# Kernel optimization log

Hardware: AMD Instinct MI355X
Metric: run time of the kernel (lower is better)

The kernel has to match this reference:

```python
import jax, jax.numpy as jnp
import numpy as np

D_MODEL = 512
N_HEADS = 8
D_HEAD = 64
D_FF = 1024
EPS = 1e-5


def setup_inputs() -> dict:
    key = jax.random.key(0)
    ks = jax.random.split(key, 9)
    B, L = 4, 2048
    s = lambda fan_in: 1.0 / np.sqrt(fan_in)
    return {
        "x": jax.random.normal(ks[0], (B, L, D_MODEL), dtype=jnp.float32),
        "ln1_w": jnp.ones((D_MODEL,), jnp.float32),
        "ln1_b": jnp.zeros((D_MODEL,), jnp.float32),
        "ln2_w": jnp.ones((D_MODEL,), jnp.float32),
        "ln2_b": jnp.zeros((D_MODEL,), jnp.float32),
        "wq": jax.random.normal(ks[1], (D_MODEL, N_HEADS * D_HEAD), jnp.float32) * s(D_MODEL),
        "wk": jax.random.normal(ks[2], (D_MODEL, N_HEADS * D_HEAD), jnp.float32) * s(D_MODEL),
        "wv": jax.random.normal(ks[3], (D_MODEL, N_HEADS * D_HEAD), jnp.float32) * s(D_MODEL),
        "wo": jax.random.normal(ks[4], (N_HEADS * D_HEAD, D_MODEL), jnp.float32) * s(N_HEADS * D_HEAD),
        "w_gate": jax.random.normal(ks[5], (D_MODEL, D_FF), jnp.float32) * s(D_MODEL),
        "w_up": jax.random.normal(ks[6], (D_MODEL, D_FF), jnp.float32) * s(D_MODEL),
        "w_down": jax.random.normal(ks[7], (D_FF, D_MODEL), jnp.float32) * s(D_FF),
    }


def _layernorm(x, w, b):
    mu = jnp.mean(x, axis=-1, keepdims=True)
    var = jnp.var(x, axis=-1, keepdims=True)
    return (x - mu) * jax.lax.rsqrt(var + EPS) * w + b


def reference(x, ln1_w, ln1_b, ln2_w, ln2_b, wq, wk, wv, wo, w_gate, w_up, w_down):
    B, L, _ = x.shape
    scale = D_HEAD ** -0.5

    # --- attention sublayer (pre-LN residual) ---
    h = _layernorm(x, ln1_w, ln1_b)
    q = (h @ wq).reshape(B, L, N_HEADS, D_HEAD)  # [B,L,H,Dh]
    k = (h @ wk).reshape(B, L, N_HEADS, D_HEAD)
    v = (h @ wv).reshape(B, L, N_HEADS, D_HEAD)
    scores = jnp.einsum("bqhd,bkhd->bhqk", q, k) * scale
    # softmax computed in fp32, cast back (matches F.softmax(dtype=float32).to(q.dtype))
    attn = jax.nn.softmax(scores.astype(jnp.float32), axis=-1).astype(q.dtype)
    out = jnp.einsum("bhqk,bkhd->bqhd", attn, v).reshape(B, L, N_HEADS * D_HEAD)
    x = x + out @ wo

    # --- SwiGLU FFN sublayer (pre-LN residual) ---
    h = _layernorm(x, ln2_w, ln2_b)
    gate = jax.nn.silu(h @ w_gate)
    x = x + (gate * (h @ w_up)) @ w_down
    return x
```

## Files before the change

### kernel.cpp

```cpp
#include <hip/hip_runtime.h>
#include <hip/hip_bf16.h>
#include <math.h>

#define EPS 1e-5f

typedef __attribute__((ext_vector_type(8))) short bf16x8;
typedef __attribute__((ext_vector_type(4))) float f32x4;
typedef __attribute__((ext_vector_type(16))) float f32x16;

#define MFMA16 __builtin_amdgcn_mfma_f32_16x16x32_bf16
#define MFMA32 __builtin_amdgcn_mfma_f32_32x32x16_bf16

__device__ __forceinline__ short f2bf(float x) {
    union { float f; unsigned u; } un; un.f = x;
    unsigned r = un.u + 0x7FFF + ((un.u >> 16) & 1);
    return (short)(r >> 16);
}
__device__ __forceinline__ float bf2f(short s) {
    union { unsigned u; float f; } un;
    un.u = ((unsigned)(unsigned short)s) << 16;
    return un.f;
}
__device__ __forceinline__ unsigned pack_bf2(float a, float b) {
    unsigned r;
    asm("v_cvt_pk_bf16_f32 %0, %1, %2" : "=v"(r) : "v"(a), "v"(b));
    return r;
}
__device__ __forceinline__ float exp2_fast(float x) {
    float r;
    asm("v_exp_f32 %0, %1" : "=v"(r) : "v"(x));
    return r;
}
__device__ __forceinline__ void permswap(unsigned& a, unsigned& b) {
    asm volatile("v_permlane32_swap_b32 %0, %1" : "+v"(a), "+v"(b));
}
__device__ __forceinline__ bf16x8 mk_frag(unsigned a, unsigned b, unsigned c, unsigned d) {
    union { unsigned u[4]; bf16x8 v; } t;
    t.u[0] = a; t.u[1] = b; t.u[2] = c; t.u[3] = d;
    return t.v;
}
__device__ __forceinline__ void load_lds16(const short* g, short* l) {
    __builtin_amdgcn_global_load_lds(
        (const __attribute__((address_space(1))) unsigned int*)g,
        (__attribute__((address_space(3))) unsigned int*)l, 16, 0, 0);
}
__device__ __forceinline__ void wait_vm0_barrier() {
    asm volatile("s_waitcnt vmcnt(0)" ::: "memory");
    __builtin_amdgcn_s_barrier();
    __builtin_amdgcn_sched_barrier(0);
}

__global__ __launch_bounds__(256) void ln_kernel_b(const float* __restrict__ in,
                                                   const float* __restrict__ w,
                                                   const float* __restrict__ bb,
                                                   short* __restrict__ out) {
    int wv = threadIdx.x >> 6, lane = threadIdx.x & 63;
    int row = blockIdx.x * 4 + wv;
    const float* x = in + (size_t)row * 512 + lane * 8;
    float4 v0 = *(const float4*)x;
    float4 v1 = *(const float4*)(x + 4);
    float s  = (v0.x + v0.y) + (v0.z + v0.w) + (v1.x + v1.y) + (v1.z + v1.w);
    float s2 = v0.x*v0.x + v0.y*v0.y + v0.z*v0.z + v0.w*v0.w
             + v1.x*v1.x + v1.y*v1.y + v1.z*v1.z + v1.w*v1.w;
#pragma unroll
    for (int off = 1; off < 64; off <<= 1) {
        s  += __shfl_xor(s, off);
        s2 += __shfl_xor(s2, off);
    }
    float mu = s * (1.f / 512.f);
    float rstd = rsqrtf(s2 * (1.f / 512.f) - mu * mu + EPS);
    const float4 wa = *(const float4*)&w[lane * 8];
    const float4 wb = *(const float4*)&w[lane * 8 + 4];
    const float4 ba = *(const float4*)&bb[lane * 8];
    const float4 bv = *(const float4*)&bb[lane * 8 + 4];
    uint4 o;
    o.x = pack_bf2((v0.x - mu) * rstd * wa.x + ba.x, (v0.y - mu) * rstd * wa.y + ba.y);
    o.y = pack_bf2((v0.z - mu) * rstd * wa.z + ba.z, (v0.w - mu) * rstd * wa.w + ba.w);
    o.z = pack_bf2((v1.x - mu) * rstd * wb.x + bv.x, (v1.y - mu) * rstd * wb.y + bv.y);
    o.w = pack_bf2((v1.z - mu) * rstd * wb.z + bv.z, (v1.w - mu) * rstd * wb.w + bv.w);
    *(uint4*)&out[(size_t)row * 512 + lane * 8] = o;
}

struct WT { const float* w; short* t; int K; int N; };
struct WT7 { WT a[7]; };
__global__ __launch_bounds__(256) void transp_w_kernel(WT7 p) {
    WT e = p.a[blockIdx.z];
    int k0 = blockIdx.x * 32, n0 = blockIdx.y * 32;
    if (k0 >= e.K || n0 >= e.N) return;
    __shared__ short t[32][33];
    int tx = threadIdx.x & 31, ty = threadIdx.x >> 5;
#pragma unroll
    for (int pp = 0; pp < 4; pp++)
        t[pp * 8 + ty][tx] = f2bf(e.w[(size_t)(k0 + pp * 8 + ty) * e.N + n0 + tx]);
    __syncthreads();
#pragma unroll
    for (int pp = 0; pp < 4; pp++)
        e.t[(size_t)(n0 + pp * 8 + ty) * e.K + k0 + tx] = t[tx][pp * 8 + ty];
}

template <int EPI, int BM, int BN>
__global__ __launch_bounds__(256) void gemm_mfma(const short* __restrict__ A,
                                                 const short* __restrict__ Bt,
                                                 const float* __restrict__ res,
                                                 const short* __restrict__ resb,
                                                 void* __restrict__ Cv,
                                                 int M, int N, int K) {
    constexpr int MI = BM >> 5;
    constexpr int NJ = BN >> 5;
    __shared__ short As[2][BM * 64];
    __shared__ short Bs[2][BN * 64];
    const int tid = threadIdx.x;
    const int lane = tid & 63, w = tid >> 6;
    const int g = lane >> 4, r16 = lane & 15;
    const int wr = w >> 1, wc = w & 1;

    const int nb = gridDim.x * gridDim.y;
    const int fid = blockIdx.y * gridDim.x + blockIdx.x;
    const int nid = (fid & 7) * (nb >> 3) + (fid >> 3);
    const int m0 = (nid / gridDim.x) * BM, n0 = (nid % gridDim.x) * BN;

    const int lr = lane >> 3;
    const int ck = (lane & 7) ^ lr;

    auto stage = [&](int buf, int k0) {
#pragma unroll
        for (int p = 0; p < BM / 32; p++) {
            int rb = w * (BM / 4) + p * 8;
            load_lds16(&A[(size_t)(m0 + rb + lr) * K + k0 + ck * 8], &As[buf][rb * 64]);
        }
#pragma unroll
        for (int p = 0; p < BN / 32; p++) {
            int rb = w * (BN / 4) + p * 8;
            load_lds16(&Bt[(size_t)(n0 + rb + lr) * K + k0 + ck * 8], &Bs[buf][rb * 64]);
        }
    };

    f32x4 acc[MI][NJ] = {};
    stage(0, 0);
    wait_vm0_barrier();

    const int nt = K >> 6;
    int cur = 0;
    for (int t = 0; t < nt; t++) {
        if (t + 1 < nt) stage(cur ^ 1, (t + 1) << 6);
#pragma unroll
        for (int ks = 0; ks < 2; ks++) {
            bf16x8 av[MI], bv[NJ];
#pragma unroll
            for (int i = 0; i < MI; i++) {
                int row = wr * (BM >> 1) + i * 16 + r16;
                av[i] = *(const bf16x8*)&As[cur][row * 64 + ((ks * 4 + g) ^ (row & 7)) * 8];
            }
#pragma unroll
            for (int j = 0; j < NJ; j++) {
                int row = wc * (BN >> 1) + j * 16 + r16;
                bv[j] = *(const bf16x8*)&Bs[cur][row * 64 + ((ks * 4 + g) ^ (row & 7)) * 8];
            }
#pragma unroll
            for (int i = 0; i < MI; i++)
#pragma unroll
                for (int j = 0; j < NJ; j++)
                    acc[i][j] = MFMA16(av[i], bv[j], acc[i][j], 0, 0, 0);
        }
        wait_vm0_barrier();
        cur ^= 1;
    }

#pragma unroll
    for (int i = 0; i < MI; i++)
#pragma unroll
        for (int j = 0; j < NJ; j++)
#pragma unroll
            for (int jr = 0; jr < 4; jr++) {
                int m = m0 + wr * (BM >> 1) + i * 16 + 4 * g + jr;
                int n = n0 + wc * (BN >> 1) + j * 16 + r16;
                float v = acc[i][j][jr];
                if (EPI == 0) {
                    size_t idx = (size_t)m * N + n;
                    ((float*)Cv)[idx] = res[idx] + v;
                } else if (EPI == 1) {
                    ((short*)Cv)[(size_t)m * N + n] = f2bf(v);
                } else if (EPI == 2) {
                    if (n < 512) v *= 0.18033688011112042f;
                    if (n < 1024) {
                        ((short*)Cv)[(size_t)(n >> 9) * 4194304 +
                                     (((size_t)(m >> 11) * 8 + ((n >> 6) & 7)) * 2048 + (m & 2047)) * 64 + (n & 63)] = f2bf(v);
                    } else {
                        ((short*)Cv)[(size_t)2 * 4194304 +
                                     (((size_t)(m >> 11) * 8 + ((n >> 6) & 7)) * 64 + (n & 63)) * 2048 + (m & 2047)] = f2bf(v);
                    }
                } else {
                    float gt = bf2f(resb[(size_t)m * N + n]);
                    float y = gt / (1.f + __expf(-gt)) * v;
                    ((short*)Cv)[(size_t)m * N + n] = f2bf(y);
                }
            }
}

__global__ __launch_bounds__(256) void attn_mfma_kernel(const short* __restrict__ qb,
                                                        const short* __restrict__ kb,
                                                        const short* __restrict__ vt,
                                                        short* __restrict__ outb) {
    __shared__ short SM[16384];

    const int fid = blockIdx.y * gridDim.x + blockIdx.x;
    const int nid = (fid & 7) * 64 + (fid >> 3);
    const int bh = nid >> 4, qt = nid & 15;
    const int b = bh >> 3, h = bh & 7;
    const int q0 = qt * 128;
    const size_t hb = (size_t)bh * (2048 * 64);

    const int tid = threadIdx.x;
    const int lane = tid & 63, w = tid >> 6;
    const int hi = lane >> 5;
    const int l31 = lane & 31;
    const int lr = lane >> 3, ck = (lane & 7) ^ lr;

#pragma unroll
    for (int p = 0; p < 4; p++)
        load_lds16(&qb[hb + (size_t)(q0 + 32 * w + 8 * p + lr) * 64 + ck * 8],
                   &SM[8192 + (32 * w + 8 * p) * 64]);
    wait_vm0_barrier();
    bf16x8 qf[4];
    {
        int row = 32 * w + l31;
#pragma unroll
        for (int ds = 0; ds < 4; ds++)
            qf[ds] = *(const bf16x8*)&SM[8192 + row * 64 + ((2 * ds + hi) ^ (row & 7)) * 8];
    }
    asm volatile("s_waitcnt lgkmcnt(0)" ::: "memory");
    __builtin_amdgcn_s_barrier();
    __builtin_amdgcn_sched_barrier(0);

    auto stageKV = [&](int buf, int kt) {
        int k0 = kt * 64;
        int rb = w * 16;
        short* Kd = &SM[buf * 4096];
        short* Vd = &SM[8192 + buf * 4096];
        load_lds16(&kb[hb + (size_t)(k0 + rb + lr) * 64 + ck * 8],       &Kd[rb * 64]);
        load_lds16(&kb[hb + (size_t)(k0 + rb + 8 + lr) * 64 + ck * 8],   &Kd[(rb + 8) * 64]);
        load_lds16(&vt[hb + (size_t)(rb + lr) * 2048 + k0 + ck * 8],     &Vd[rb * 64]);
        load_lds16(&vt[hb + (size_t)(rb + 8 + lr) * 2048 + k0 + ck * 8], &Vd[(rb + 8) * 64]);
    };
    stageKV(0, 0);
    wait_vm0_barrier();

    float m_ = -1e30f, l_ = 0.f;
    f32x16 o0 = (f32x16)(0.f), o1 = (f32x16)(0.f);
    int cur = 0;

    for (int t = 0; t < 32; t++) {
        if (t + 1 < 32) stageKV(cur ^ 1, t + 1);
        const short* Kc = &SM[cur * 4096];
        const short* Vc = &SM[8192 + cur * 4096];

        f32x16 s0 = (f32x16)(0.f), s1 = (f32x16)(0.f);
        {
            int r0 = l31, r1 = 32 + l31;
            int cshift = (l31 & 7);
#pragma unroll
            for (int ds = 0; ds < 4; ds++) {
                bf16x8 k0f = *(const bf16x8*)&Kc[r0 * 64 + ((2 * ds + hi) ^ cshift) * 8];
                bf16x8 k1f = *(const bf16x8*)&Kc[r1 * 64 + ((2 * ds + hi) ^ cshift) * 8];
                s0 = MFMA32(k0f, qf[ds], s0, 0, 0, 0);
                s1 = MFMA32(k1f, qf[ds], s1, 0, 0, 0);
            }
        }

        float q0m = fmaxf(fmaxf(s0[0], s0[1]),  fmaxf(s0[2], s0[3]));
        float q1m = fmaxf(fmaxf(s0[4], s0[5]),  fmaxf(s0[6], s0[7]));
        float q2m = fmaxf(fmaxf(s0[8], s0[9]),  fmaxf(s0[10], s0[11]));
        float q3m = fmaxf(fmaxf(s0[12], s0[13]), fmaxf(s0[14], s0[15]));
        float q4m = fmaxf(fmaxf(s1[0], s1[1]),  fmaxf(s1[2], s1[3]));
        float q5m = fmaxf(fmaxf(s1[4], s1[5]),  fmaxf(s1[6], s1[7]));
        float q6m = fmaxf(fmaxf(s1[8], s1[9]),  fmaxf(s1[10], s1[11]));
        float q7m = fmaxf(fmaxf(s1[12], s1[13]), fmaxf(s1[14], s1[15]));
        float om = fmaxf(fmaxf(fmaxf(q0m, q1m), fmaxf(q2m, q3m)),
                         fmaxf(fmaxf(q4m, q5m), fmaxf(q6m, q7m)));
        unsigned ua = __float_as_uint(om), ub = ua;
        permswap(ua, ub);
        float pm = fmaxf(__uint_as_float(ua), __uint_as_float(ub));

        if (!__all(pm - m_ <= 8.f)) {
            float mn = fmaxf(m_, pm);
            float al = exp2_fast(m_ - mn);
            l_ *= al;
            o0 *= al;
            o1 *= al;
            m_ = mn;
        }

        float rs = 0.f;
#pragma unroll
        for (int r = 0; r < 16; r++) { s0[r] = exp2_fast(s0[r] - m_); rs += s0[r]; }
#pragma unroll
        for (int r = 0; r < 16; r++) { s1[r] = exp2_fast(s1[r] - m_); rs += s1[r]; }
        l_ += rs;

        bf16x8 pf[4];
#pragma unroll
        for (int ks = 0; ks < 2; ks++) {
            unsigned X0 = pack_bf2(s0[8 * ks + 0], s0[8 * ks + 1]);
            unsigned X1 = pack_bf2(s0[8 * ks + 2], s0[8 * ks + 3]);
            unsigned Y0 = pack_bf2(s0[8 * ks + 4], s0[8 * ks + 5]);
            unsigned Y1 = pack_bf2(s0[8 * ks + 6], s0[8 * ks + 7]);
            permswap(X0, Y0);
            permswap(X1, Y1);
            pf[ks] = mk_frag(X0, X1, Y0, Y1);
        }
#pragma unroll
        for (int ks = 0; ks < 2; ks++) {
            unsigned X0 = pack_bf2(s1[8 * ks + 0], s1[8 * ks + 1]);
            unsigned X1 = pack_bf2(s1[8 * ks + 2], s1[8 * ks + 3]);
            unsigned Y0 = pack_bf2(s1[8 * ks + 4], s1[8 * ks + 5]);
            unsigned Y1 = pack_bf2(s1[8 * ks + 6], s1[8 * ks + 7]);
            permswap(X0, Y0);
            permswap(X1, Y1);
            pf[2 + ks] = mk_frag(X0, X1, Y0, Y1);
        }

        {
            int r0 = l31, r1 = 32 + l31;
            int cs0 = r0 & 7, cs1 = r1 & 7;
#pragma unroll
            for (int kk = 0; kk < 4; kk++) {
                int kc = 2 * kk + hi;
                bf16x8 v0f = *(const bf16x8*)&Vc[r0 * 64 + (kc ^ cs0) * 8];
                bf16x8 v1f = *(const bf16x8*)&Vc[r1 * 64 + (kc ^ cs1) * 8];
                o0 = MFMA32(v0f, pf[kk], o0, 0, 0, 0);
                o1 = MFMA32(v1f, pf[kk], o1, 0, 0, 0);
            }
        }

        wait_vm0_barrier();
        cur ^= 1;
    }

    unsigned sa = __float_as_uint(l_), sb = sa;
    permswap(sa, sb);
    float inv = 1.f / (__uint_as_float(sa) + __uint_as_float(sb));
    int q = q0 + 32 * w + l31;
    size_t obase = ((size_t)b * 2048 + q) * 512 + h * 64;
#pragma unroll
    for (int rr = 0; rr < 4; rr++) {
        int d0 = 8 * rr + 4 * hi;
        unsigned long long pv =
            (unsigned long long)pack_bf2(o0[4 * rr + 0] * inv, o0[4 * rr + 1] * inv)
          | ((unsigned long long)pack_bf2(o0[4 * rr + 2] * inv, o0[4 * rr + 3] * inv) << 32);
        *(unsigned long long*)&outb[obase + d0] = pv;
        unsigned long long pv2 =
            (unsigned long long)pack_bf2(o1[4 * rr + 0] * inv, o1[4 * rr + 1] * inv)
          | ((unsigned long long)pack_bf2(o1[4 * rr + 2] * inv, o1[4 * rr + 3] * inv) << 32);
        *(unsigned long long*)&outb[obase + 32 + d0] = pv2;
    }
}

extern "C" void kernel_launch(void* const* d_in, const int* in_sizes, int n_in,
                              void* d_out, int out_size, void* d_ws, size_t ws_size,
                              hipStream_t stream) {
    const float* x      = (const float*)d_in[0];
    const float* ln1_w  = (const float*)d_in[1];
    const float* ln1_b  = (const float*)d_in[2];
    const float* ln2_w  = (const float*)d_in[3];
    const float* ln2_b  = (const float*)d_in[4];
    const float* wq     = (const float*)d_in[5];
    const float* wk     = (const float*)d_in[6];
    const float* wv     = (const float*)d_in[7];
    const float* wo     = (const float*)d_in[8];
    const float* w_gate = (const float*)d_in[9];
    const float* w_up   = (const float*)d_in[10];
    const float* w_down = (const float*)d_in[11];
    float* out = (float*)d_out;

    const int M = 4 * 2048;
    char* ws = (char*)d_ws;
    const size_t MB = 1 << 20;
    short* h1b   = (short*)(ws);
    short* qb    = (short*)(ws + 8 * MB);
    short* kb    = (short*)(ws + 16 * MB);
    short* vt    = (short*)(ws + 24 * MB);
    short* aob   = (short*)(ws + 40 * MB);
    short* g_b   = (short*)(ws + 48 * MB);
    short* u_b   = (short*)(ws + 64 * MB);
    short* qkvT  = (short*)(ws + 80 * MB);
    short* woT   = (short*)(ws + 82 * MB);
    short* wguT  = (short*)(ws + 83 * MB);
    short* wdT   = (short*)(ws + 85 * MB);
    short* h2b   = qb;

    WT7 wt;
    wt.a[0] = {wq,     qkvT,               512,  512};
    wt.a[1] = {wk,     qkvT + 512 * 512,   512,  512};
    wt.a[2] = {wv,     qkvT + 1024 * 512,  512,  512};
    wt.a[3] = {wo,     woT,                512,  512};
    wt.a[4] = {w_gate, wguT,               512, 1024};
    wt.a[5] = {w_up,   wguT + 1024 * 512,  512, 1024};
    wt.a[6] = {w_down, wdT,               1024,  512};

    transp_w_kernel<<<dim3(32, 32, 7), 256, 0, stream>>>(wt);
    ln_kernel_b<<<M / 4, 256, 0, stream>>>(x, ln1_w, ln1_b, h1b);
    gemm_mfma<2, 64, 128><<<dim3(12, 128), 256, 0, stream>>>(h1b, qkvT, nullptr, nullptr, qb, M, 1536, 512);
    attn_mfma_kernel<<<dim3(16, 32), 256, 0, stream>>>(qb, kb, vt, aob);
    gemm_mfma<0, 64, 64><<<dim3(8, 128), 256, 0, stream>>>(aob, woT, x, nullptr, out, M, 512, 512);
    ln_kernel_b<<<M / 4, 256, 0, stream>>>(out, ln2_w, ln2_b, h2b);
    gemm_mfma<1, 64, 128><<<dim3(8, 128), 256, 0, stream>>>(h2b, wguT, nullptr, nullptr, g_b, M, 1024, 512);
    gemm_mfma<4, 64, 128><<<dim3(8, 128), 256, 0, stream>>>(h2b, wguT + 1024 * 512, nullptr, g_b, u_b, M, 1024, 512);
    gemm_mfma<0, 64, 64><<<dim3(8, 128), 256, 0, stream>>>(u_b, wdT, out, nullptr, out, M, 512, 1024);
}
```

Before: 177.9 us.

## Fuse gate/up GEMMs with SwiGLU epilogue, separate V transpose, enlarge GEMM tiles

Merges the gate and up projections into one kernel that accumulates both products from a shared A tile and applies SiLU-multiply in registers. This removes the bf16 gate intermediate round-trip and one A-operand read. The QKV GEMM now writes V untransposed, and a separate LDS-tiled kernel transposes it, replacing the scattered strided store in the epilogue. The QKV, out-projection and down-projection GEMMs switch from 64-row to 128-row tiles, halving the grid. The cost is an extra launch, extra traffic for the V transpose, and lower occupancy from larger tiles.

```diff
diff --git a/kernel.cpp b/kernel.cpp
--- a/kernel.cpp
+++ b/kernel.cpp
@@ -102,7 +102,6 @@
 __global__ __launch_bounds__(256) void gemm_mfma(const short* __restrict__ A,
                                                  const short* __restrict__ Bt,
                                                  const float* __restrict__ res,
-                                                 const short* __restrict__ resb,
                                                  void* __restrict__ Cv,
                                                  int M, int N, int K) {
     constexpr int MI = BM >> 5;
@@ -178,23 +177,124 @@
                 if (EPI == 0) {
                     size_t idx = (size_t)m * N + n;
                     ((float*)Cv)[idx] = res[idx] + v;
-                } else if (EPI == 1) {
-                    ((short*)Cv)[(size_t)m * N + n] = f2bf(v);
-                } else if (EPI == 2) {
+                } else {
                     if (n < 512) v *= 0.18033688011112042f;
-                    if (n < 1024) {
-                        ((short*)Cv)[(size_t)(n >> 9) * 4194304 +
-                                     (((size_t)(m >> 11) * 8 + ((n >> 6) & 7)) * 2048 + (m & 2047)) * 64 + (n & 63)] = f2bf(v);
-                    } else {
-                        ((short*)Cv)[(size_t)2 * 4194304 +
-                                     (((size_t)(m >> 11) * 8 + ((n >> 6) & 7)) * 64 + (n & 63)) * 2048 + (m & 2047)] = f2bf(v);
-                    }
-                } else {
-                    float gt = bf2f(resb[(size_t)m * N + n]);
-                    float y = gt / (1.f + __expf(-gt)) * v;
-                    ((short*)Cv)[(size_t)m * N + n] = f2bf(y);
+                    ((short*)Cv)[(size_t)(n >> 9) * 4194304 +
+                                 (((size_t)(m >> 11) * 8 + ((n >> 6) & 7)) * 2048 + (m & 2047)) * 64 + (n & 63)] = f2bf(v);
                 }
             }
+}
+
+__global__ __launch_bounds__(256) void ffn_gateup_kernel(const short* __restrict__ A,
+                                                         const short* __restrict__ Bg,
+                                                         const short* __restrict__ Bu,
+                                                         short* __restrict__ U,
+                                                         int M, int N, int K) {
+    constexpr int BM = 128, BN = 64;
+    constexpr int MI = 4, NJ = 2;
+    __shared__ short As[2][BM * 64];
+    __shared__ short Bgs[2][BN * 64];
+    __shared__ short Bus[2][BN * 64];
+    const int tid = threadIdx.x;
+    const int lane = tid & 63, w = tid >> 6;
+    const int g = lane >> 4, r16 = lane & 15;
+    const int wr = w >> 1, wc = w & 1;
+
+    const int nb = gridDim.x * gridDim.y;
+    const int fid = blockIdx.y * gridDim.x + blockIdx.x;
+    const int nid = (fid & 7) * (nb >> 3) + (fid >> 3);
+    const int m0 = (nid / gridDim.x) * BM, n0 = (nid % gridDim.x) * BN;
+
+    const int lr = lane >> 3;
+    const int ck = (lane & 7) ^ lr;
+
+    auto stage = [&](int buf, int k0) {
+#pragma unroll
+        for (int p = 0; p < 4; p++) {
+            int rb = w * 32 + p * 8;
+            load_lds16(&A[(size_t)(m0 + rb + lr) * K + k0 + ck * 8], &As[buf][rb * 64]);
+        }
+#pragma unroll
+        for (int p = 0; p < 2; p++) {
+            int rb = w * 16 + p * 8;
+            load_lds16(&Bg[(size_t)(n0 + rb + lr) * K + k0 + ck * 8], &Bgs[buf][rb * 64]);
+            load_lds16(&Bu[(size_t)(n0 + rb + lr) * K + k0 + ck * 8], &Bus[buf][rb * 64]);
+        }
+    };
+
+    f32x4 accg[MI][NJ] = {};
+    f32x4 accu[MI][NJ] = {};
+    stage(0, 0);
+    wait_vm0_barrier();
+
+    const int nt = K >> 6;
+    int cur = 0;
+    for (int t = 0; t < nt; t++) {
+        if (t + 1 < nt) stage(cur ^ 1, (t + 1) << 6);
+#pragma unroll
+        for (int ks = 0; ks < 2; ks++) {
+            bf16x8 av[MI], bgv[NJ], buv[NJ];
+#pragma unroll
+            for (int i = 0; i < MI; i++) {
+                int row = wr * 64 + i * 16 + r16;
+                av[i] = *(const bf16x8*)&As[cur][row * 64 + ((ks * 4 + g) ^ (row & 7)) * 8];
+            }
+#pragma unroll
+            for (int j = 0; j < NJ; j++) {
+                int row = wc * 32 + j * 16 + r16;
+                int off = row * 64 + ((ks * 4 + g) ^ (row & 7)) * 8;
+                bgv[j] = *(const bf16x8*)&Bgs[cur][off];
+                buv[j] = *(const bf16x8*)&Bus[cur][off];
+            }
+#pragma unroll
+            for (int i = 0; i < MI; i++)
+#pragma unroll
+                for (int j = 0; j < NJ; j++) {
+                    accg[i][j] = MFMA16(av[i], bgv[j], accg[i][j], 0, 0, 0);
+                    accu[i][j] = MFMA16(av[i], buv[j], accu[i][j], 0, 0, 0);
+                }
+        }
+        wait_vm0_barrier();
+        cur ^= 1;
+    }
+
+#pragma unroll
+    for (int i = 0; i < MI; i++)
+#pragma unroll
+        for (int j = 0; j < NJ; j++)
+#pragma unroll
+            for (int jr = 0; jr < 4; jr++) {
+                int m = m0 + wr * 64 + i * 16 + 4 * g + jr;
+                int n = n0 + wc * 32 + j * 16 + r16;
+                float gt = accg[i][j][jr];
+                float y = gt / (1.f + __expf(-gt)) * accu[i][j][jr];
+                U[(size_t)m * N + n] = f2bf(y);
+            }
+}
+
+__global__ __launch_bounds__(256) void transp_v_kernel(const short* __restrict__ vb,
+                                                       short* __restrict__ vt) {
+    __shared__ short tile[64][65];
+    int l0 = blockIdx.x * 64;
+    int bh = blockIdx.y;
+    const size_t base = (size_t)bh * 2048 * 64;
+    int tid = threadIdx.x;
+#pragma unroll
+    for (int p = 0; p < 4; p++) {
+        int r = p * 16 + (tid >> 4);
+        int c4 = (tid & 15) * 4;
+        *(short4*)&tile[r][c4] = *(const short4*)&vb[base + (size_t)(l0 + r) * 64 + c4];
+    }
+    __syncthreads();
+#pragma unroll
+    for (int p = 0; p < 4; p++) {
+        int d = p * 16 + (tid >> 4);
+        int c4 = (tid & 15) * 4;
+        short4 o;
+        o.x = tile[c4 + 0][d]; o.y = tile[c4 + 1][d];
+        o.z = tile[c4 + 2][d]; o.w = tile[c4 + 3][d];
+        *(short4*)&vt[base + (size_t)d * 2048 + l0 + c4] = o;
+    }
 }
 
 __global__ __launch_bounds__(256) void attn_mfma_kernel(const short* __restrict__ qb,
@@ -378,10 +478,10 @@
     short* h1b   = (short*)(ws);
     short* qb    = (short*)(ws + 8 * MB);
     short* kb    = (short*)(ws + 16 * MB);
-    short* vt    = (short*)(ws + 24 * MB);
+    short* vb    = (short*)(ws + 24 * MB);
+    short* vt    = (short*)(ws + 32 * MB);
     short* aob   = (short*)(ws + 40 * MB);
-    short* g_b   = (short*)(ws + 48 * MB);
-    short* u_b   = (short*)(ws + 64 * MB);
+    short* u_b   = (short*)(ws + 48 * MB);
     short* qkvT  = (short*)(ws + 80 * MB);
     short* woT   = (short*)(ws + 82 * MB);
     short* wguT  = (short*)(ws + 83 * MB);
@@ -399,11 +499,11 @@
 
     transp_w_kernel<<<dim3(32, 32, 7), 256, 0, stream>>>(wt);
     ln_kernel_b<<<M / 4, 256, 0, stream>>>(x, ln1_w, ln1_b, h1b);
-    gemm_mfma<2, 64, 128><<<dim3(12, 128), 256, 0, stream>>>(h1b, qkvT, nullptr, nullptr, qb, M, 1536, 512);
+    gemm_mfma<2, 128, 128><<<dim3(12, 64), 256, 0, stream>>>(h1b, qkvT, nullptr, qb, M, 1536, 512);
+    transp_v_kernel<<<dim3(32, 32), 256, 0, stream>>>(vb, vt);
     attn_mfma_kernel<<<dim3(16, 32), 256, 0, stream>>>(qb, kb, vt, aob);
-    gemm_mfma<0, 64, 64><<<dim3(8, 128), 256, 0, stream>>>(aob, woT, x, nullptr, out, M, 512, 512);
+    gemm_mfma<0, 128, 64><<<dim3(8, 64), 256, 0, stream>>>(aob, woT, x, out, M, 512, 512);
     ln_kernel_b<<<M / 4, 256, 0, stream>>>(out, ln2_w, ln2_b, h2b);
-    gemm_mfma<1, 64, 128><<<dim3(8, 128), 256, 0, stream>>>(h2b, wguT, nullptr, nullptr, g_b, M, 1024, 512);
-    gemm_mfma<4, 64, 128><<<dim3(8, 128), 256, 0, stream>>>(h2b, wguT + 1024 * 512, nullptr, g_b, u_b, M, 1024, 512);
-    gemm_mfma<0, 64, 64><<<dim3(8, 128), 256, 0, stream>>>(u_b, wdT, out, nullptr, out, M, 512, 1024);
-}
+    ffn_gateup_kernel<<<dim3(16, 64), 256, 0, stream>>>(h2b, wguT, wguT + 1024 * 512, u_b, M, 1024, 512);
+    gemm_mfma<0, 128, 64><<<dim3(8, 64), 256, 0, stream>>>(u_b, wdT, out, out, M, 512, 1024);
+}
```

Result: faster. 155.8 us (-12.4%).
